# Optimization experiments

Measured on AMD Instinct MI355X. Metric: run time of the kernel, lower is better.

The kernel has to match this reference:

```python
import jax, jax.numpy as jnp
import numpy as np

N_HEAD = 16

def setup_inputs() -> dict:
    key = jax.random.key(0)
    k1, k2, k3 = jax.random.split(key, 3)
    B, S, D = 2, 2048, 1024
    x = jax.random.normal(k1, (B, S, D), dtype=jnp.float32)
    w_attn = jax.random.normal(k2, (D, 3 * D), dtype=jnp.float32) * 0.02
    b_attn = jnp.zeros((3 * D,), dtype=jnp.float32)
    w_proj = jax.random.normal(k3, (D, D), dtype=jnp.float32) * 0.02
    b_proj = jnp.zeros((D,), dtype=jnp.float32)
    return {"x": x, "w_attn": w_attn, "b_attn": b_attn, "w_proj": w_proj, "b_proj": b_proj}

def reference(x, w_attn, b_attn, w_proj, b_proj):
    B, S, D = x.shape
    hd = D // N_HEAD
    qkv = x @ w_attn + b_attn                      # [B,S,3D]
    q, k, v = jnp.split(qkv, 3, axis=-1)
    def heads(t):  # [B,S,D] -> [B,H,S,hd]
        return t.reshape(B, S, N_HEAD, hd).transpose(0, 2, 1, 3)
    q, k, v = heads(q), heads(k), heads(v)
    # NOTE: original forward applies NO scaling and NO causal mask; dropout=eval (identity)
    scores = jnp.einsum('bhqd,bhkd->bhqk', q, k)   # [B,H,S,S]
    probs = jax.nn.softmax(scores, axis=-1)
    out = jnp.einsum('bhqk,bhkd->bhqd', probs, v)  # [B,H,S,hd]
    out = out.transpose(0, 2, 1, 3).reshape(B, S, D)
    return out @ w_proj + b_proj
```

## Files before the change

### kernel.cpp

```cpp
#include <hip/hip_runtime.h>

typedef _Float16 f16;
typedef _Float16 f16x8 __attribute__((ext_vector_type(8)));
typedef _Float16 f16x4 __attribute__((ext_vector_type(4)));
typedef float    f32x4 __attribute__((ext_vector_type(4)));
typedef unsigned int u32;
typedef unsigned int u32x4 __attribute__((ext_vector_type(4)));

#define LOG2E 1.44269504088896340736f
#define EXPC  (13.0f * 1.44269504088896340736f)

__device__ __forceinline__ void gload_lds16(const void* g, void* l) {
  __builtin_amdgcn_global_load_lds(
      (const __attribute__((address_space(1))) void*)g,
      (__attribute__((address_space(3))) void*)l, 16, 0, 0);
}

__device__ __forceinline__ void block_sync() {
  asm volatile("" ::: "memory");
  __builtin_amdgcn_s_barrier();
  asm volatile("" ::: "memory");
}

__global__ __launch_bounds__(256)
void k_prep(const float* __restrict__ x, f16* __restrict__ xh,
            const float* __restrict__ w_attn, f16* __restrict__ waT,
            const float* __restrict__ w_proj, f16* __restrict__ wpT) {
  __shared__ float tile[32][33];
  const int bid = blockIdx.x;
  const int t = threadIdx.x;
  if (bid < 4096) {
    int i = bid * 256 + t;
    f32x4 v = ((const f32x4*)x)[i];
    f16x4 o;
    o[0] = (f16)v[0]; o[1] = (f16)v[1]; o[2] = (f16)v[2]; o[3] = (f16)v[3];
    ((f16x4*)xh)[i] = o;
    return;
  }
  const float* in; f16* out; int R, C, bx, by;
  if (bid < 4096 + 3072) {
    int q = bid - 4096; in = w_attn; out = waT; R = 1024; C = 3072;
    bx = q % 96; by = q / 96;
  } else {
    int q = bid - 7168; in = w_proj; out = wpT; R = 1024; C = 1024;
    bx = q % 32; by = q / 32;
  }
  int tx = t & 31, ty = t >> 5;
  int c0 = bx * 32, r0 = by * 32;
#pragma unroll
  for (int i = 0; i < 4; i++)
    tile[ty + i * 8][tx] = in[(size_t)(r0 + ty + i * 8) * C + c0 + tx];
  __syncthreads();
#pragma unroll
  for (int i = 0; i < 4; i++)
    out[(size_t)(c0 + ty + i * 8) * R + r0 + tx] = (f16)tile[tx][ty + i * 8];
}

template <int EPI>
__global__ __launch_bounds__(256)
void k_gemm(const f16* __restrict__ A, const f16* __restrict__ BT,
            const float* __restrict__ bias,
            f16* __restrict__ out_qk, f16* __restrict__ out_vT,
            float* __restrict__ out_f) {
  constexpr int K = 1024;
  __shared__ f16 smem[4][128 * 64];
  const int t = threadIdx.x;
  const int l = t & 63;
  const int w = t >> 6;
  const int wm = (w >> 1) * 64;
  const int wn = (w & 1) * 64;
  const int m0 = blockIdx.x * 128;
  const int n0 = blockIdx.y * 128;
  const int lr = l & 15;
  const int lg = l >> 4;
  const int fr8 = lr & 7;

  const int row8g = t >> 3;
  const int scg = (t & 7) ^ (row8g & 7);
  const f16* Ap = A + (size_t)(m0 + row8g) * K + scg * 8;
  const f16* Bp = BT + (size_t)(n0 + row8g) * K + scg * 8;

#define GSTAGE(buf) do { \
    _Pragma("unroll") \
    for (int i2 = 0; i2 < 4; i2++) \
      gload_lds16(Ap + (size_t)(i2 * 32) * K, &smem[buf][(i2 * 256 + t) * 8]); \
    _Pragma("unroll") \
    for (int i2 = 0; i2 < 4; i2++) \
      gload_lds16(Bp + (size_t)(i2 * 32) * K, &smem[2 + buf][(i2 * 256 + t) * 8]); \
    Ap += 64; Bp += 64; } while (0)

  f32x4 acc[4][4] = {};

#define GCOMPUTE(buf) do { \
    _Pragma("unroll") \
    for (int kk = 0; kk < 64; kk += 32) { \
      const int cbase = (kk >> 3) + lg; \
      f16x8 af[4], bf[4]; \
      _Pragma("unroll") \
      for (int i = 0; i < 4; i++) \
        af[i] = *(const f16x8*)&smem[buf][((wm + i * 16 + lr) * 8 + (cbase ^ fr8)) * 8]; \
      _Pragma("unroll") \
      for (int j = 0; j < 4; j++) \
        bf[j] = *(const f16x8*)&smem[2 + buf][((wn + j * 16 + lr) * 8 + (cbase ^ fr8)) * 8]; \
      _Pragma("unroll") \
      for (int i = 0; i < 4; i++) \
        _Pragma("unroll") \
        for (int j = 0; j < 4; j++) \
          acc[i][j] = __builtin_amdgcn_mfma_f32_16x16x32_f16(af[i], bf[j], acc[i][j], 0, 0, 0); \
    } } while (0)

  GSTAGE(0);
  asm volatile("s_waitcnt vmcnt(0)" ::: "memory");
  block_sync();

  for (int kt = 0; kt < 16; kt += 2) {
    GSTAGE(1);
    GCOMPUTE(0);
    asm volatile("s_waitcnt vmcnt(0)" ::: "memory");
    block_sync();
    if (kt + 2 < 16) GSTAGE(0);
    GCOMPUTE(1);
    asm volatile("s_waitcnt vmcnt(0)" ::: "memory");
    block_sync();
  }
#undef GSTAGE
#undef GCOMPUTE

  if (EPI == 1) {
#pragma unroll
    for (int i = 0; i < 4; i++) {
      int mbase = m0 + wm + i * 16 + (l >> 4) * 4;
#pragma unroll
      for (int j = 0; j < 4; j++) {
        int n = n0 + wn + j * 16 + lr;
        float bv = bias[n];
#pragma unroll
        for (int r = 0; r < 4; r++)
          out_f[(size_t)(mbase + r) * 1024 + n] = acc[i][j][r] + bv;
      }
    }
  } else if (n0 < 2048) {
#pragma unroll
    for (int i = 0; i < 4; i++) {
      int mbase = m0 + wm + i * 16 + (l >> 4) * 4;
#pragma unroll
      for (int j = 0; j < 4; j++) {
        int n = n0 + wn + j * 16 + lr;
        float bv = bias[n];
        float sc = (n0 + wn + j * 16 < 1024) ? LOG2E : 1.0f;
#pragma unroll
        for (int r = 0; r < 4; r++)
          out_qk[(size_t)(mbase + r) * 2048 + n] = (f16)((acc[i][j][r] + bv) * sc);
      }
    }
  } else {
    f16* scr = &smem[0][0];
#pragma unroll
    for (int i = 0; i < 4; i++) {
      int s0 = wm + i * 16 + (l >> 4) * 4;
#pragma unroll
      for (int j = 0; j < 4; j++) {
        int nl = wn + j * 16 + lr;
        float bv = bias[n0 + nl];
        f16x4 pv;
#pragma unroll
        for (int r = 0; r < 4; r++) pv[r] = (f16)(acc[i][j][r] + bv);
        *(f16x4*)&scr[nl * 128 + (s0 ^ ((nl & 15) << 3))] = pv;
      }
    }
    block_sync();
    const int b = m0 >> 11;
    const int kvc0 = (m0 & 2047) >> 3;
    const int h0 = (n0 - 2048) >> 6;
    const int l64 = t & 63;
    const int wv = t >> 6;
#pragma unroll
    for (int p = 0; p < 8; p++) {
      int pair = wv + p * 4;
      int kvcl = pair & 15;
      int hgl  = pair >> 4;
      int nl = hgl * 64 + l64;
      f16x8 vv = *(const f16x8*)&scr[nl * 128 + ((kvcl * 8) ^ ((nl & 15) << 3))];
      size_t dst = (((size_t)(b * 16 + h0 + hgl) * 256 + kvc0 + kvcl) * 64 + l64) * 8;
      *(f16x8*)&out_vT[dst] = vv;
    }
  }
}

__global__ __launch_bounds__(256, 4)
void k_attn(const f16* __restrict__ qk, const f16* __restrict__ vT,
            f16* __restrict__ aout) {
  __shared__ f16 Kl[2][64 * 64];
  const int t = threadIdx.x;
  const int l = t & 63;
  const int w = t >> 6;
  const int lr = l & 15;
  const int lg = l >> 4;
  const int lk = lg * 8;

  const int o  = (blockIdx.x & 7) * 128 + (blockIdx.x >> 3);
  const int qt = o & 31;
  const int bh = o >> 5;
  const int b  = bh >> 4;
  const int h  = bh & 15;
  const int q0 = qt * 64 + w * 16;

  const f16* qp = qk + (size_t)(b * 2048 + q0 + lr) * 2048 + h * 64 + lk;
  f16x8 qf0 = *(const f16x8*)qp;
  f16x8 qf1 = *(const f16x8*)(qp + 32);

  const f16* kg = qk + (size_t)(b * 2048) * 2048 + 1024 + h * 64;
  const int row8 = t >> 3;
  const int off0 = row8 * 2048 + (((t & 7) ^ (row8 & 7)) << 3);
  const int off1 = off0 + 32 * 2048;

  const f16* vg0 = vT + (((size_t)bh * 256 + lg) * 64 + lr) * 8;

#define STAGE(B) do { \
    gload_lds16(kg + off0, &Kl[B][t * 8]); \
    gload_lds16(kg + off1, &Kl[B][(256 + t) * 8]); \
    kg += 64 * 2048; } while (0)

  f32x4 oa[4] = {};
  f32x4 ssum = {};
  const f32x4 initc = {-EXPC, -EXPC, -EXPC, -EXPC};
  f16x8 ones;
#pragma unroll
  for (int j = 0; j < 8; j++) ones[j] = (f16)1.0f;

  STAGE(0);
  asm volatile("s_waitcnt vmcnt(0)" ::: "memory");
  block_sync();

#define TILE_BODY(B) do { \
    f16x8 vfr[4][2]; \
    _Pragma("unroll") \
    for (int c4 = 0; c4 < 4; c4++) \
      _Pragma("unroll") \
      for (int ks = 0; ks < 2; ks++) \
        vfr[c4][ks] = *(const f16x8*)(vg0 + ks * 2048 + c4 * 128); \
    f32x4 sa[4]; \
    __builtin_amdgcn_s_setprio(1); \
    _Pragma("unroll") \
    for (int c = 0; c < 4; c++) { \
      const int ks = c >> 1, cc = c & 1; \
      const int row = ks * 32 + (lr >> 2) * 8 + (lr & 3) * 2 + cc; \
      const int r7 = row & 7; \
      f16x8 kf0 = *(const f16x8*)&Kl[B][(row * 8 + (lg ^ r7)) * 8]; \
      f16x8 kf1 = *(const f16x8*)&Kl[B][(row * 8 + ((lg + 4) ^ r7)) * 8]; \
      sa[c] = __builtin_amdgcn_mfma_f32_16x16x32_f16(kf0, qf0, initc, 0, 0, 0); \
      sa[c] = __builtin_amdgcn_mfma_f32_16x16x32_f16(kf1, qf1, sa[c], 0, 0, 0); \
    } \
    __builtin_amdgcn_s_setprio(0); \
    _Pragma("unroll") \
    for (int c = 0; c < 4; c++) \
      _Pragma("unroll") \
      for (int r = 0; r < 4; r++) \
        sa[c][r] = exp2f(sa[c][r]); \
    u32 pka[2][4]; \
    _Pragma("unroll") \
    for (int ks = 0; ks < 2; ks++) \
      _Pragma("unroll") \
      for (int u = 0; u < 4; u++) \
        pka[ks][u] = __builtin_bit_cast(u32, \
            __builtin_amdgcn_cvt_pkrtz(sa[2 * ks][u], sa[2 * ks + 1][u])); \
    f16x8 pa0 = __builtin_bit_cast(f16x8, (u32x4){pka[0][0], pka[0][1], pka[0][2], pka[0][3]}); \
    f16x8 pa1 = __builtin_bit_cast(f16x8, (u32x4){pka[1][0], pka[1][1], pka[1][2], pka[1][3]}); \
    __builtin_amdgcn_s_setprio(1); \
    ssum = __builtin_amdgcn_mfma_f32_16x16x32_f16(pa0, ones, ssum, 0, 0, 0); \
    ssum = __builtin_amdgcn_mfma_f32_16x16x32_f16(pa1, ones, ssum, 0, 0, 0); \
    _Pragma("unroll") \
    for (int c4 = 0; c4 < 4; c4++) { \
      oa[c4] = __builtin_amdgcn_mfma_f32_16x16x32_f16(pa0, vfr[c4][0], oa[c4], 0, 0, 0); \
      oa[c4] = __builtin_amdgcn_mfma_f32_16x16x32_f16(pa1, vfr[c4][1], oa[c4], 0, 0, 0); \
    } \
    __builtin_amdgcn_s_setprio(0); \
    vg0 += 4096; \
    asm volatile("s_waitcnt vmcnt(0)" ::: "memory"); \
    block_sync(); } while (0)

  for (int tt = 0; tt < 32; tt += 2) {
    STAGE(1);
    TILE_BODY(0);
    if (tt + 2 < 32) STAGE(0);
    TILE_BODY(1);
  }
#undef STAGE
#undef TILE_BODY

#pragma unroll
  for (int r = 0; r < 4; r++) {
    float ia = 1.0f / ssum[r];
    size_t rowa = (size_t)(b * 2048 + q0 + lg * 4 + r);
#pragma unroll
    for (int c4 = 0; c4 < 4; c4++)
      aout[rowa * 1024 + h * 64 + c4 * 16 + lr] = (f16)(oa[c4][r] * ia);
  }
}

extern "C" void kernel_launch(void* const* d_in, const int* in_sizes, int n_in,
                              void* d_out, int out_size, void* d_ws, size_t ws_size,
                              hipStream_t stream) {
  const float* x      = (const float*)d_in[0];
  const float* w_attn = (const float*)d_in[1];
  const float* b_attn = (const float*)d_in[2];
  const float* w_proj = (const float*)d_in[3];
  const float* b_proj = (const float*)d_in[4];
  float* out = (float*)d_out;

  char* p = (char*)d_ws;
  f16* xh  = (f16*)p;  p += (size_t)4096 * 1024 * 2;
  f16* waT = (f16*)p;  p += (size_t)3072 * 1024 * 2;
  f16* wpT = (f16*)p;  p += (size_t)1024 * 1024 * 2;
  f16* qkb = (f16*)p;  p += (size_t)4096 * 2048 * 2;
  f16* vTb = (f16*)p;  p += (size_t)32 * 256 * 64 * 8 * 2;
  f16* aob = (f16*)p;  p += (size_t)4096 * 1024 * 2;
  if ((size_t)(p - (char*)d_ws) > ws_size) return;

  k_prep<<<8192, 256, 0, stream>>>(x, xh, w_attn, waT, w_proj, wpT);
  k_gemm<0><<<dim3(32, 24), 256, 0, stream>>>(xh, waT, b_attn, qkb, vTb, nullptr);
  k_attn<<<1024, 256, 0, stream>>>(qkb, vTb, aob);
  k_gemm<1><<<dim3(32, 8), 256, 0, stream>>>(aob, wpT, b_proj, nullptr, nullptr, out);
}
```

Before: 118.7 us.

## Double KV tile to 128 rows per iteration in attention kernel

Doubles the K tile staged in LDS from 64 to 128 keys per iteration, so the loop runs half as many times and has half as many barriers and vmcnt waits. The key-row permutation moves from the LDS read side to the global-load side, and the fast exp2 builtin replaces exp2f. LDS use doubles to 32KB per block and register pressure rises from the extra V fragments and score registers, which may hurt occupancy at the requested 4 blocks per CU.

```diff
diff --git a/kernel.cpp b/kernel.cpp
--- a/kernel.cpp
+++ b/kernel.cpp
@@ -190,13 +190,14 @@
 __global__ __launch_bounds__(256, 4)
 void k_attn(const f16* __restrict__ qk, const f16* __restrict__ vT,
             f16* __restrict__ aout) {
-  __shared__ f16 Kl[2][64 * 64];
+  __shared__ f16 Kl[2][128 * 64];
   const int t = threadIdx.x;
   const int l = t & 63;
   const int w = t >> 6;
   const int lr = l & 15;
   const int lg = l >> 4;
   const int lk = lg * 8;
+  const int r7 = lr & 7;
 
   const int o  = (blockIdx.x & 7) * 128 + (blockIdx.x >> 3);
   const int qt = o & 31;
@@ -210,16 +211,19 @@
   f16x8 qf1 = *(const f16x8*)(qp + 32);
 
   const f16* kg = qk + (size_t)(b * 2048) * 2048 + 1024 + h * 64;
-  const int row8 = t >> 3;
-  const int off0 = row8 * 2048 + (((t & 7) ^ (row8 & 7)) << 3);
-  const int off1 = off0 + 32 * 2048;
+  const int r5 = t >> 3;
+  const int u_s = r5 & 15;
+  const int prow = (u_s >> 2) * 8 + (u_s & 3) * 2 + (r5 >> 4);
+  const int sc_s = ((t & 7) ^ (r5 & 7)) << 3;
 
   const f16* vg0 = vT + (((size_t)bh * 256 + lg) * 64 + lr) * 8;
 
 #define STAGE(B) do { \
-    gload_lds16(kg + off0, &Kl[B][t * 8]); \
-    gload_lds16(kg + off1, &Kl[B][(256 + t) * 8]); \
-    kg += 64 * 2048; } while (0)
+    gload_lds16(kg + (size_t)(prow     ) * 2048 + sc_s, &Kl[B][(      t) * 8]); \
+    gload_lds16(kg + (size_t)(prow + 32) * 2048 + sc_s, &Kl[B][(256 + t) * 8]); \
+    gload_lds16(kg + (size_t)(prow + 64) * 2048 + sc_s, &Kl[B][(512 + t) * 8]); \
+    gload_lds16(kg + (size_t)(prow + 96) * 2048 + sc_s, &Kl[B][(768 + t) * 8]); \
+    kg += 128 * 2048; } while (0)
 
   f32x4 oa[4] = {};
   f32x4 ssum = {};
@@ -233,56 +237,73 @@
   block_sync();
 
 #define TILE_BODY(B) do { \
-    f16x8 vfr[4][2]; \
+    f16x8 vfrA[4][2]; \
     _Pragma("unroll") \
     for (int c4 = 0; c4 < 4; c4++) \
       _Pragma("unroll") \
       for (int ks = 0; ks < 2; ks++) \
-        vfr[c4][ks] = *(const f16x8*)(vg0 + ks * 2048 + c4 * 128); \
-    f32x4 sa[4]; \
+        vfrA[c4][ks] = *(const f16x8*)(vg0 + ks * 2048 + c4 * 128); \
+    f16x8 pa[4]; \
+    _Pragma("unroll") \
+    for (int hh = 0; hh < 2; hh++) { \
+      f32x4 sa[4]; \
+      __builtin_amdgcn_s_setprio(1); \
+      _Pragma("unroll") \
+      for (int cc2 = 0; cc2 < 4; cc2++) { \
+        const int c = hh * 4 + cc2; \
+        const int ks = c >> 1, cc = c & 1; \
+        const int row = ks * 32 + cc * 16 + lr; \
+        f16x8 kf0 = *(const f16x8*)&Kl[B][(row * 8 + (lg ^ r7)) * 8]; \
+        f16x8 kf1 = *(const f16x8*)&Kl[B][(row * 8 + ((lg + 4) ^ r7)) * 8]; \
+        sa[cc2] = __builtin_amdgcn_mfma_f32_16x16x32_f16(kf0, qf0, initc, 0, 0, 0); \
+        sa[cc2] = __builtin_amdgcn_mfma_f32_16x16x32_f16(kf1, qf1, sa[cc2], 0, 0, 0); \
+      } \
+      __builtin_amdgcn_s_setprio(0); \
+      _Pragma("unroll") \
+      for (int cc2 = 0; cc2 < 4; cc2++) \
+        _Pragma("unroll") \
+        for (int r = 0; r < 4; r++) \
+          sa[cc2][r] = __builtin_amdgcn_exp2f(sa[cc2][r]); \
+      u32 pk[2][4]; \
+      _Pragma("unroll") \
+      for (int k2 = 0; k2 < 2; k2++) \
+        _Pragma("unroll") \
+        for (int u = 0; u < 4; u++) \
+          pk[k2][u] = __builtin_bit_cast(u32, \
+              __builtin_amdgcn_cvt_pkrtz(sa[2 * k2][u], sa[2 * k2 + 1][u])); \
+      pa[hh * 2 + 0] = __builtin_bit_cast(f16x8, (u32x4){pk[0][0], pk[0][1], pk[0][2], pk[0][3]}); \
+      pa[hh * 2 + 1] = __builtin_bit_cast(f16x8, (u32x4){pk[1][0], pk[1][1], pk[1][2], pk[1][3]}); \
+    } \
+    f16x8 vfrB[4][2]; \
+    _Pragma("unroll") \
+    for (int c4 = 0; c4 < 4; c4++) \
+      _Pragma("unroll") \
+      for (int ks = 0; ks < 2; ks++) \
+        vfrB[c4][ks] = *(const f16x8*)(vg0 + (2 + ks) * 2048 + c4 * 128); \
     __builtin_amdgcn_s_setprio(1); \
-    _Pragma("unroll") \
-    for (int c = 0; c < 4; c++) { \
-      const int ks = c >> 1, cc = c & 1; \
-      const int row = ks * 32 + (lr >> 2) * 8 + (lr & 3) * 2 + cc; \
-      const int r7 = row & 7; \
-      f16x8 kf0 = *(const f16x8*)&Kl[B][(row * 8 + (lg ^ r7)) * 8]; \
-      f16x8 kf1 = *(const f16x8*)&Kl[B][(row * 8 + ((lg + 4) ^ r7)) * 8]; \
-      sa[c] = __builtin_amdgcn_mfma_f32_16x16x32_f16(kf0, qf0, initc, 0, 0, 0); \
-      sa[c] = __builtin_amdgcn_mfma_f32_16x16x32_f16(kf1, qf1, sa[c], 0, 0, 0); \
+    ssum = __builtin_amdgcn_mfma_f32_16x16x32_f16(pa[0], ones, ssum, 0, 0, 0); \
+    ssum = __builtin_amdgcn_mfma_f32_16x16x32_f16(pa[1], ones, ssum, 0, 0, 0); \
+    ssum = __builtin_amdgcn_mfma_f32_16x16x32_f16(pa[2], ones, ssum, 0, 0, 0); \
+    ssum = __builtin_amdgcn_mfma_f32_16x16x32_f16(pa[3], ones, ssum, 0, 0, 0); \
+    _Pragma("unroll") \
+    for (int c4 = 0; c4 < 4; c4++) { \
+      oa[c4] = __builtin_amdgcn_mfma_f32_16x16x32_f16(pa[0], vfrA[c4][0], oa[c4], 0, 0, 0); \
+      oa[c4] = __builtin_amdgcn_mfma_f32_16x16x32_f16(pa[1], vfrA[c4][1], oa[c4], 0, 0, 0); \
+    } \
+    _Pragma("unroll") \
+    for (int c4 = 0; c4 < 4; c4++) { \
+      oa[c4] = __builtin_amdgcn_mfma_f32_16x16x32_f16(pa[2], vfrB[c4][0], oa[c4], 0, 0, 0); \
+      oa[c4] = __builtin_amdgcn_mfma_f32_16x16x32_f16(pa[3], vfrB[c4][1], oa[c4], 0, 0, 0); \
     } \
     __builtin_amdgcn_s_setprio(0); \
-    _Pragma("unroll") \
-    for (int c = 0; c < 4; c++) \
-      _Pragma("unroll") \
-      for (int r = 0; r < 4; r++) \
-        sa[c][r] = exp2f(sa[c][r]); \
-    u32 pka[2][4]; \
-    _Pragma("unroll") \
-    for (int ks = 0; ks < 2; ks++) \
-      _Pragma("unroll") \
-      for (int u = 0; u < 4; u++) \
-        pka[ks][u] = __builtin_bit_cast(u32, \
-            __builtin_amdgcn_cvt_pkrtz(sa[2 * ks][u], sa[2 * ks + 1][u])); \
-    f16x8 pa0 = __builtin_bit_cast(f16x8, (u32x4){pka[0][0], pka[0][1], pka[0][2], pka[0][3]}); \
-    f16x8 pa1 = __builtin_bit_cast(f16x8, (u32x4){pka[1][0], pka[1][1], pka[1][2], pka[1][3]}); \
-    __builtin_amdgcn_s_setprio(1); \
-    ssum = __builtin_amdgcn_mfma_f32_16x16x32_f16(pa0, ones, ssum, 0, 0, 0); \
-    ssum = __builtin_amdgcn_mfma_f32_16x16x32_f16(pa1, ones, ssum, 0, 0, 0); \
-    _Pragma("unroll") \
-    for (int c4 = 0; c4 < 4; c4++) { \
-      oa[c4] = __builtin_amdgcn_mfma_f32_16x16x32_f16(pa0, vfr[c4][0], oa[c4], 0, 0, 0); \
-      oa[c4] = __builtin_amdgcn_mfma_f32_16x16x32_f16(pa1, vfr[c4][1], oa[c4], 0, 0, 0); \
-    } \
-    __builtin_amdgcn_s_setprio(0); \
-    vg0 += 4096; \
+    vg0 += 8192; \
     asm volatile("s_waitcnt vmcnt(0)" ::: "memory"); \
     block_sync(); } while (0)
 
-  for (int tt = 0; tt < 32; tt += 2) {
+  for (int tt = 0; tt < 16; tt += 2) {
     STAGE(1);
     TILE_BODY(0);
-    if (tt + 2 < 32) STAGE(0);
+    if (tt + 2 < 16) STAGE(0);
     TILE_BODY(1);
   }
 #undef STAGE
```

Result: slower. 144.4 us (+21.7%).

## Emit K in MFMA fragment order from QKV GEMM and drop LDS staging in attention

Applied to the files above, without the earlier changes.

The QKV GEMM epilogue now writes K into a separate buffer pre-permuted into the per-lane MFMA fragment layout, so the attention kernel can load K fragments straight from global memory with coalesced 16-byte loads. This removes the LDS double buffering, async global-to-LDS copies, waitcnt and block barriers from the attention loop. Each wave now fetches K from global/L2 on its own instead of sharing one LDS tile across the block, and the loads are no longer explicitly overlapped with compute. exp2f is also swapped for the hardware exp2 builtin.

```diff
diff --git a/kernel.cpp b/kernel.cpp
--- a/kernel.cpp
+++ b/kernel.cpp
@@ -60,8 +60,8 @@
 __global__ __launch_bounds__(256)
 void k_gemm(const f16* __restrict__ A, const f16* __restrict__ BT,
             const float* __restrict__ bias,
-            f16* __restrict__ out_qk, f16* __restrict__ out_vT,
-            float* __restrict__ out_f) {
+            f16* __restrict__ out_qk, f16* __restrict__ out_kb,
+            f16* __restrict__ out_vT, float* __restrict__ out_f) {
   constexpr int K = 1024;
   __shared__ f16 smem[4][128 * 64];
   const int t = threadIdx.x;
@@ -139,7 +139,7 @@
           out_f[(size_t)(mbase + r) * 1024 + n] = acc[i][j][r] + bv;
       }
     }
-  } else if (n0 < 2048) {
+  } else if (n0 < 1024) {
 #pragma unroll
     for (int i = 0; i < 4; i++) {
       int mbase = m0 + wm + i * 16 + (l >> 4) * 4;
@@ -147,10 +147,9 @@
       for (int j = 0; j < 4; j++) {
         int n = n0 + wn + j * 16 + lr;
         float bv = bias[n];
-        float sc = (n0 + wn + j * 16 < 1024) ? LOG2E : 1.0f;
 #pragma unroll
         for (int r = 0; r < 4; r++)
-          out_qk[(size_t)(mbase + r) * 2048 + n] = (f16)((acc[i][j][r] + bv) * sc);
+          out_qk[(size_t)(mbase + r) * 2048 + n] = (f16)((acc[i][j][r] + bv) * LOG2E);
       }
     }
   } else {
@@ -170,27 +169,52 @@
     }
     block_sync();
     const int b = m0 >> 11;
-    const int kvc0 = (m0 & 2047) >> 3;
-    const int h0 = (n0 - 2048) >> 6;
-    const int l64 = t & 63;
-    const int wv = t >> 6;
-#pragma unroll
-    for (int p = 0; p < 8; p++) {
-      int pair = wv + p * 4;
-      int kvcl = pair & 15;
-      int hgl  = pair >> 4;
-      int nl = hgl * 64 + l64;
-      f16x8 vv = *(const f16x8*)&scr[nl * 128 + ((kvcl * 8) ^ ((nl & 15) << 3))];
-      size_t dst = (((size_t)(b * 16 + h0 + hgl) * 256 + kvc0 + kvcl) * 64 + l64) * 8;
-      *(f16x8*)&out_vT[dst] = vv;
+    if (n0 < 2048) {
+      const int Sg0 = (m0 & 2047) >> 5;
+      const int h0 = (n0 - 1024) >> 6;
+      const int kbi = t >> 3;
+      const int li = t & 7;
+      const int hf   = kbi & 1;
+      const int cc   = (kbi >> 1) & 1;
+      const int S_l  = (kbi >> 2) & 3;
+      const int bh_l = kbi >> 4;
+      size_t kbidx = ((((size_t)(b * 16 + h0 + bh_l) * 64 + Sg0 + S_l) * 2 + cc) * 2 + hf);
+      f16* dst = out_kb + kbidx * 512;
+#pragma unroll
+      for (int e = 0; e < 8; e++) {
+        int lp = li * 8 + e;
+        int s = S_l * 32 + 2 * (lp & 15) + cc;
+        int nlb = bh_l * 64 + (hf * 4 + (lp >> 4)) * 8;
+        f16x8 vv;
+#pragma unroll
+        for (int j = 0; j < 8; j++) {
+          int nl = nlb + j;
+          vv[j] = scr[nl * 128 + (s ^ ((nl & 15) << 3))];
+        }
+        *(f16x8*)&dst[lp * 8] = vv;
+      }
+    } else {
+      const int kvc0 = (m0 & 2047) >> 3;
+      const int h0 = (n0 - 2048) >> 6;
+      const int l64 = t & 63;
+      const int wv = t >> 6;
+#pragma unroll
+      for (int p = 0; p < 8; p++) {
+        int pair = wv + p * 4;
+        int kvcl = pair & 15;
+        int hgl  = pair >> 4;
+        int nl = hgl * 64 + l64;
+        f16x8 vv = *(const f16x8*)&scr[nl * 128 + ((kvcl * 8) ^ ((nl & 15) << 3))];
+        size_t dst = (((size_t)(b * 16 + h0 + hgl) * 256 + kvc0 + kvcl) * 64 + l64) * 8;
+        *(f16x8*)&out_vT[dst] = vv;
+      }
     }
   }
 }
 
 __global__ __launch_bounds__(256, 4)
-void k_attn(const f16* __restrict__ qk, const f16* __restrict__ vT,
-            f16* __restrict__ aout) {
-  __shared__ f16 Kl[2][64 * 64];
+void k_attn(const f16* __restrict__ qk, const f16* __restrict__ kb,
+            const f16* __restrict__ vT, f16* __restrict__ aout) {
   const int t = threadIdx.x;
   const int l = t & 63;
   const int w = t >> 6;
@@ -209,17 +233,8 @@
   f16x8 qf0 = *(const f16x8*)qp;
   f16x8 qf1 = *(const f16x8*)(qp + 32);
 
-  const f16* kg = qk + (size_t)(b * 2048) * 2048 + 1024 + h * 64;
-  const int row8 = t >> 3;
-  const int off0 = row8 * 2048 + (((t & 7) ^ (row8 & 7)) << 3);
-  const int off1 = off0 + 32 * 2048;
-
+  const f16* kbp = kb + (size_t)bh * 131072 + l * 8;
   const f16* vg0 = vT + (((size_t)bh * 256 + lg) * 64 + lr) * 8;
-
-#define STAGE(B) do { \
-    gload_lds16(kg + off0, &Kl[B][t * 8]); \
-    gload_lds16(kg + off1, &Kl[B][(256 + t) * 8]); \
-    kg += 64 * 2048; } while (0)
 
   f32x4 oa[4] = {};
   f32x4 ssum = {};
@@ -228,65 +243,52 @@
 #pragma unroll
   for (int j = 0; j < 8; j++) ones[j] = (f16)1.0f;
 
-  STAGE(0);
-  asm volatile("s_waitcnt vmcnt(0)" ::: "memory");
-  block_sync();
-
-#define TILE_BODY(B) do { \
-    f16x8 vfr[4][2]; \
-    _Pragma("unroll") \
-    for (int c4 = 0; c4 < 4; c4++) \
-      _Pragma("unroll") \
-      for (int ks = 0; ks < 2; ks++) \
-        vfr[c4][ks] = *(const f16x8*)(vg0 + ks * 2048 + c4 * 128); \
-    f32x4 sa[4]; \
-    __builtin_amdgcn_s_setprio(1); \
-    _Pragma("unroll") \
-    for (int c = 0; c < 4; c++) { \
-      const int ks = c >> 1, cc = c & 1; \
-      const int row = ks * 32 + (lr >> 2) * 8 + (lr & 3) * 2 + cc; \
-      const int r7 = row & 7; \
-      f16x8 kf0 = *(const f16x8*)&Kl[B][(row * 8 + (lg ^ r7)) * 8]; \
-      f16x8 kf1 = *(const f16x8*)&Kl[B][(row * 8 + ((lg + 4) ^ r7)) * 8]; \
-      sa[c] = __builtin_amdgcn_mfma_f32_16x16x32_f16(kf0, qf0, initc, 0, 0, 0); \
-      sa[c] = __builtin_amdgcn_mfma_f32_16x16x32_f16(kf1, qf1, sa[c], 0, 0, 0); \
-    } \
-    __builtin_amdgcn_s_setprio(0); \
-    _Pragma("unroll") \
-    for (int c = 0; c < 4; c++) \
-      _Pragma("unroll") \
-      for (int r = 0; r < 4; r++) \
-        sa[c][r] = exp2f(sa[c][r]); \
-    u32 pka[2][4]; \
-    _Pragma("unroll") \
-    for (int ks = 0; ks < 2; ks++) \
-      _Pragma("unroll") \
-      for (int u = 0; u < 4; u++) \
-        pka[ks][u] = __builtin_bit_cast(u32, \
-            __builtin_amdgcn_cvt_pkrtz(sa[2 * ks][u], sa[2 * ks + 1][u])); \
-    f16x8 pa0 = __builtin_bit_cast(f16x8, (u32x4){pka[0][0], pka[0][1], pka[0][2], pka[0][3]}); \
-    f16x8 pa1 = __builtin_bit_cast(f16x8, (u32x4){pka[1][0], pka[1][1], pka[1][2], pka[1][3]}); \
-    __builtin_amdgcn_s_setprio(1); \
-    ssum = __builtin_amdgcn_mfma_f32_16x16x32_f16(pa0, ones, ssum, 0, 0, 0); \
-    ssum = __builtin_amdgcn_mfma_f32_16x16x32_f16(pa1, ones, ssum, 0, 0, 0); \
-    _Pragma("unroll") \
-    for (int c4 = 0; c4 < 4; c4++) { \
-      oa[c4] = __builtin_amdgcn_mfma_f32_16x16x32_f16(pa0, vfr[c4][0], oa[c4], 0, 0, 0); \
-      oa[c4] = __builtin_amdgcn_mfma_f32_16x16x32_f16(pa1, vfr[c4][1], oa[c4], 0, 0, 0); \
-    } \
-    __builtin_amdgcn_s_setprio(0); \
-    vg0 += 4096; \
-    asm volatile("s_waitcnt vmcnt(0)" ::: "memory"); \
-    block_sync(); } while (0)
-
-  for (int tt = 0; tt < 32; tt += 2) {
-    STAGE(1);
-    TILE_BODY(0);
-    if (tt + 2 < 32) STAGE(0);
-    TILE_BODY(1);
-  }
-#undef STAGE
-#undef TILE_BODY
+  for (int tt = 0; tt < 32; tt++) {
+    f16x8 vfr[4][2];
+#pragma unroll
+    for (int c4 = 0; c4 < 4; c4++)
+#pragma unroll
+      for (int ks = 0; ks < 2; ks++)
+        vfr[c4][ks] = *(const f16x8*)(vg0 + ks * 2048 + c4 * 128);
+
+    f32x4 sa[4];
+    __builtin_amdgcn_s_setprio(1);
+#pragma unroll
+    for (int c = 0; c < 4; c++) {
+      const int ks = c >> 1, cc = c & 1;
+      f16x8 kf0 = *(const f16x8*)(kbp + (4 * ks + 2 * cc + 0) * 512);
+      f16x8 kf1 = *(const f16x8*)(kbp + (4 * ks + 2 * cc + 1) * 512);
+      sa[c] = __builtin_amdgcn_mfma_f32_16x16x32_f16(kf0, qf0, initc, 0, 0, 0);
+      sa[c] = __builtin_amdgcn_mfma_f32_16x16x32_f16(kf1, qf1, sa[c], 0, 0, 0);
+    }
+    __builtin_amdgcn_s_setprio(0);
+#pragma unroll
+    for (int c = 0; c < 4; c++)
+#pragma unroll
+      for (int r = 0; r < 4; r++)
+        sa[c][r] = __builtin_amdgcn_exp2f(sa[c][r]);
+    u32 pka[2][4];
+#pragma unroll
+    for (int ks = 0; ks < 2; ks++)
+#pragma unroll
+      for (int u = 0; u < 4; u++)
+        pka[ks][u] = __builtin_bit_cast(u32,
+            __builtin_amdgcn_cvt_pkrtz(sa[2 * ks][u], sa[2 * ks + 1][u]));
+    f16x8 pa0 = __builtin_bit_cast(f16x8, (u32x4){pka[0][0], pka[0][1], pka[0][2], pka[0][3]});
+    f16x8 pa1 = __builtin_bit_cast(f16x8, (u32x4){pka[1][0], pka[1][1], pka[1][2], pka[1][3]});
+    __builtin_amdgcn_s_setprio(1);
+    ssum = __builtin_amdgcn_mfma_f32_16x16x32_f16(pa0, ones, ssum, 0, 0, 0);
+    ssum = __builtin_amdgcn_mfma_f32_16x16x32_f16(pa1, ones, ssum, 0, 0, 0);
+#pragma unroll
+    for (int c4 = 0; c4 < 4; c4++) {
+      oa[c4] = __builtin_amdgcn_mfma_f32_16x16x32_f16(pa0, vfr[c4][0], oa[c4], 0, 0, 0);
+      oa[c4] = __builtin_amdgcn_mfma_f32_16x16x32_f16(pa1, vfr[c4][1], oa[c4], 0, 0, 0);
+    }
+    __builtin_amdgcn_s_setprio(0);
+
+    kbp += 4096;
+    vg0 += 4096;
+  }
 
 #pragma unroll
   for (int r = 0; r < 4; r++) {
@@ -314,11 +316,12 @@
   f16* wpT = (f16*)p;  p += (size_t)1024 * 1024 * 2;
   f16* qkb = (f16*)p;  p += (size_t)4096 * 2048 * 2;
   f16* vTb = (f16*)p;  p += (size_t)32 * 256 * 64 * 8 * 2;
+  f16* kbb = (f16*)p;  p += (size_t)32 * 131072 * 2;
   f16* aob = (f16*)p;  p += (size_t)4096 * 1024 * 2;
   if ((size_t)(p - (char*)d_ws) > ws_size) return;
 
   k_prep<<<8192, 256, 0, stream>>>(x, xh, w_attn, waT, w_proj, wpT);
-  k_gemm<0><<<dim3(32, 24), 256, 0, stream>>>(xh, waT, b_attn, qkb, vTb, nullptr);
-  k_attn<<<1024, 256, 0, stream>>>(qkb, vTb, aob);
-  k_gemm<1><<<dim3(32, 8), 256, 0, stream>>>(aob, wpT, b_proj, nullptr, nullptr, out);
-}
+  k_gemm<0><<<dim3(32, 24), 256, 0, stream>>>(xh, waT, b_attn, qkb, kbb, vTb, nullptr);
+  k_attn<<<1024, 256, 0, stream>>>(qkb, kbb, vTb, aob);
+  k_gemm<1><<<dim3(32, 8), 256, 0, stream>>>(aob, wpT, b_proj, nullptr, nullptr, nullptr, out);
+}
```

New measurement: 126.6 us. +6.7%, slower.
